# Optimization experiments

Hardware: AMD Instinct MI355X
Metric: run time of the kernel (lower is better)

Reference implementation:

```python
import jax, jax.numpy as jnp
import numpy as np

REG_WEIGHT = 1e-4
N_LAYERS = 3


def setup_inputs() -> dict:
    key = jax.random.key(0)
    ks = jax.random.split(key, 7)
    n_users, n_items, d = 100000, 50000, 64
    E, B = 1600000, 4096
    return {
        "user_table": jax.random.normal(ks[0], (n_users, d), dtype=jnp.float32) * 0.01,
        "item_table": jax.random.normal(ks[1], (n_items, d), dtype=jnp.float32) * 0.01,
        "edge_u": jax.random.randint(ks[2], (E,), 0, n_users, dtype=jnp.int32),
        "edge_i": jax.random.randint(ks[3], (E,), 0, n_items, dtype=jnp.int32),
        "users": jax.random.randint(ks[4], (B,), 0, n_users, dtype=jnp.int32),
        "pos_items": jax.random.randint(ks[5], (B,), 0, n_items, dtype=jnp.int32),
        "neg_items": jax.random.randint(ks[6], (B,), 0, n_items, dtype=jnp.int32),
    }


def _lightgcn_embeddings(user_table, item_table, edge_u, edge_i):
    n_users, n_items = user_table.shape[0], item_table.shape[0]
    N = n_users + n_items
    E = edge_u.shape[0]
    ones = jnp.ones((E,), dtype=user_table.dtype)
    # symmetric normalization D^{-1/2} A D^{-1/2} on the bipartite graph
    deg_u = jax.ops.segment_sum(ones, edge_u, num_segments=n_users)
    deg_i = jax.ops.segment_sum(ones, edge_i, num_segments=n_items)
    w = jax.lax.rsqrt(jnp.maximum(deg_u[edge_u] * deg_i[edge_i], 1.0))
    # symmetric edge list over the stacked [users; items] node set
    rows = jnp.concatenate([edge_u, edge_i + n_users])
    cols = jnp.concatenate([edge_i + n_users, edge_u])
    vals = jnp.concatenate([w, w])[:, None]

    x = jnp.concatenate([user_table, item_table], axis=0)  # [N, d]
    acc = x
    for _ in range(N_LAYERS):
        x = jax.ops.segment_sum(x[cols] * vals, rows, num_segments=N)
        acc = acc + x
    final = acc / jnp.asarray(N_LAYERS + 1, dtype=x.dtype)
    return final[:n_users], final[n_users:]


def reference(user_table, item_table, edge_u, edge_i, users, pos_items, neg_items):
    user_emb_all, item_emb_all = _lightgcn_embeddings(user_table, item_table, edge_u, edge_i)
    u_emb = user_emb_all[users]
    pos_i_emb = item_emb_all[pos_items]
    neg_i_emb = item_emb_all[neg_items]
    pos_scores = jnp.sum(u_emb * pos_i_emb, axis=-1)
    neg_scores = jnp.sum(u_emb * neg_i_emb, axis=-1)
    # L2 regularization on the layer-0 (table) embeddings
    u0 = user_table[users]
    p0 = item_table[pos_items]
    n0 = item_table[neg_items]
    reg_loss = REG_WEIGHT * (jnp.sum(u0 * u0) + jnp.sum(p0 * p0) + jnp.sum(n0 * n0))
    reg_loss = reg_loss / users.shape[0]
    return pos_scores, neg_scores, reg_loss
```

## Files before the change

### kernel.cpp

```cpp
#include <hip/hip_runtime.h>
#include <hip/hip_fp16.h>

#define THREADS 256
#define BIN_C 4096
#define NBMAX 400
#define CAP 4608
#define SH_U 8
#define SH_I 7
#define CPAD 16
#define T_TILES 8
#define TSH_U 13
#define TSH_I 14

__global__ void bin_kernel(const int* __restrict__ eu, const int* __restrict__ ei,
                           int* __restrict__ bcnt_u, int* __restrict__ bcnt_i,
                           int* __restrict__ binu, int* __restrict__ bini,
                           int E, int nbu, int nbi) {
    __shared__ int hist_u[NBMAX], hist_i[NBMAX];
    __shared__ int base_u[NBMAX], base_i[NBMAX];
    int tid = threadIdx.x;
    int e0 = blockIdx.x * BIN_C;
    if (e0 >= E) return;
    int cnt = min(BIN_C, E - e0);

    for (int b = tid; b < NBMAX; b += THREADS) { hist_u[b] = 0; hist_i[b] = 0; }
    __syncthreads();

    int u[16], v[16];
    #pragma unroll
    for (int j = 0; j < 16; ++j) {
        int k = tid + j * THREADS;
        if (k < cnt) { u[j] = eu[e0 + k]; v[j] = ei[e0 + k]; }
        else         { u[j] = -1; v[j] = -1; }
    }
    #pragma unroll
    for (int j = 0; j < 16; ++j) {
        if (u[j] >= 0) {
            atomicAdd(&hist_u[u[j] >> SH_U], 1);
            atomicAdd(&hist_i[v[j] >> SH_I], 1);
        }
    }
    __syncthreads();
    for (int b = tid; b < NBMAX; b += THREADS) {
        int cu = hist_u[b], ci = hist_i[b];
        base_u[b] = (cu > 0 && b < nbu) ? atomicAdd(&bcnt_u[(size_t)b * CPAD], cu) : 0;
        base_i[b] = (ci > 0 && b < nbi) ? atomicAdd(&bcnt_i[(size_t)b * CPAD], ci) : 0;
        hist_u[b] = 0; hist_i[b] = 0;
    }
    __syncthreads();
    #pragma unroll
    for (int j = 0; j < 16; ++j) {
        if (u[j] >= 0) {
            int bu = u[j] >> SH_U;
            int pu = base_u[bu] + atomicAdd(&hist_u[bu], 1);
            if (pu < CAP) binu[(size_t)bu * CAP + pu] = ((u[j] & 255) << 16) | v[j];
            int bi = v[j] >> SH_I;
            int pi = base_i[bi] + atomicAdd(&hist_i[bi], 1);
            if (pi < CAP) bini[(size_t)bi * CAP + pi] = ((v[j] & 127) << 17) | u[j];
        }
    }
}

__global__ void bucket_off(const int* __restrict__ bcnt, int* __restrict__ bo,
                           int* __restrict__ cursor, int nb, int pad) {
    int idx = blockIdx.x * blockDim.x + threadIdx.x;
    int lane = threadIdx.x & 63;
    int d = 0;
    if (idx < nb) d = min(bcnt[(size_t)idx * CPAD], CAP) + pad;
    int s = d;
    #pragma unroll
    for (int ofs = 1; ofs < 64; ofs <<= 1) {
        int t = __shfl_up(s, ofs);
        if (lane >= ofs) s += t;
    }
    int total = __shfl(s, 63);
    int base = 0;
    if (lane == 63) base = atomicAdd(cursor, total);
    base = __shfl(base, 63);
    if (idx < nb) bo[idx] = base + s - d;
}

__global__ void place(const int* __restrict__ bcnt_u, const int* __restrict__ bcnt_i,
                      const int* __restrict__ bo_u, const int* __restrict__ bo_i,
                      const int* __restrict__ binu, const int* __restrict__ bini,
                      int* __restrict__ offu, int* __restrict__ offi,
                      int* __restrict__ du, int* __restrict__ di,
                      float* __restrict__ rsdu, float* __restrict__ rsdi,
                      int* __restrict__ entu, int* __restrict__ enti,
                      int nbu, int nU, int nI) {
    __shared__ int stash[CAP];
    __shared__ int bin_cnt[THREADS * T_TILES];
    __shared__ int scan[THREADS];
    __shared__ int node_base[THREADS];
    int b = blockIdx.x;
    bool isU = (b < nbu);
    const int* bin; int base_node, nn, count, bob;
    int *off, *deg, *ent; float* rsd;
    int losh, tsh, lomask;
    if (isU) {
        bin = binu + (size_t)b * CAP;
        base_node = b << SH_U; nn = min(256, nU - base_node);
        count = min(bcnt_u[(size_t)b * CPAD], CAP); bob = bo_u[b];
        off = offu; deg = du; rsd = rsdu; ent = entu;
        losh = 16; tsh = TSH_U; lomask = 0xFFFF;
    } else {
        int b2 = b - nbu;
        bin = bini + (size_t)b2 * CAP;
        base_node = b2 << SH_I; nn = min(128, nI - base_node);
        count = min(bcnt_i[(size_t)b2 * CPAD], CAP); bob = bo_i[b2];
        off = offi; deg = di; rsd = rsdi; ent = enti;
        losh = 17; tsh = TSH_I; lomask = 0x1FFFF;
    }
    int tid = threadIdx.x;
    #pragma unroll
    for (int t = 0; t < T_TILES; ++t) bin_cnt[tid + t * THREADS] = 0;
    __syncthreads();
    for (int k = tid; k < count; k += THREADS) {
        int p = bin[k];
        stash[k] = p;
        int key = ((p >> losh) << 3) | ((p & lomask) >> tsh);
        atomicAdd(&bin_cnt[key], 1);
    }
    __syncthreads();
    int c = 0;
    {
        int base = tid * T_TILES;
        #pragma unroll
        for (int t = 0; t < T_TILES; ++t) {
            int v = bin_cnt[base + t];
            bin_cnt[base + t] = c;
            c += v;
        }
    }
    int seg = (c + 15) & ~15;
    scan[tid] = seg;
    __syncthreads();
    #pragma unroll
    for (int ofs = 1; ofs < THREADS; ofs <<= 1) {
        int t = (tid >= ofs) ? scan[tid - ofs] : 0;
        __syncthreads();
        scan[tid] += t;
        __syncthreads();
    }
    int excl = scan[tid] - seg;
    node_base[tid] = excl;
    if (tid < nn) {
        off[base_node + tid] = bob + excl;
        deg[base_node + tid] = c;
        rsd[base_node + tid] = rsqrtf(fmaxf((float)c, 1.0f));
    }
    __syncthreads();
    #pragma unroll
    for (int t = 0; t < T_TILES; ++t) {
        int k = tid + t * THREADS;
        bin_cnt[k] += node_base[k >> 3];
    }
    __syncthreads();
    for (int k = tid; k < count; k += THREADS) {
        int p = stash[k];
        int key = ((p >> losh) << 3) | ((p & lomask) >> tsh);
        int sl = atomicAdd(&bin_cnt[key], 1);
        ent[bob + sl] = p & lomask;
    }
}

__global__ void conv16(const float* __restrict__ src, __half* __restrict__ dst, int n4) {
    int stride = gridDim.x * blockDim.x;
    for (int i = blockIdx.x * blockDim.x + threadIdx.x; i < n4; i += stride) {
        float4 v = *reinterpret_cast<const float4*>(src + (size_t)i * 4);
        __half2 h0 = __float22half2_rn(make_float2(v.x, v.y));
        __half2 h1 = __float22half2_rn(make_float2(v.z, v.w));
        uint2 st;
        st.x = *reinterpret_cast<unsigned*>(&h0);
        st.y = *reinterpret_cast<unsigned*>(&h1);
        *reinterpret_cast<uint2*>(dst + (size_t)i * 4) = st;
    }
}

__global__ void prop16(const __half* __restrict__ x,
                       const int* __restrict__ offu, const int* __restrict__ offi,
                       const int* __restrict__ du, const int* __restrict__ di,
                       const float* __restrict__ rsdu, const float* __restrict__ rsdi,
                       const int* __restrict__ entu, const int* __restrict__ enti,
                       __half* __restrict__ y, int nU, int N) {
    int node = blockIdx.x * (THREADS >> 3) + (threadIdx.x >> 3);
    int lane = threadIdx.x & 7;
    if (node >= N) return;
    const int* ent; const __half* src; const float* rsdn;
    int beg, dg; float rs;
    if (node < nU) {
        beg = offu[node]; dg = du[node]; rs = rsdu[node];
        ent = entu; src = x + ((size_t)nU << 6); rsdn = rsdi;
    } else {
        int i = node - nU;
        beg = offi[i]; dg = di[i]; rs = rsdi[i];
        ent = enti; src = x; rsdn = rsdu;
    }
    float a0=0,a1=0,a2=0,a3=0,a4=0,a5=0,a6=0,a7=0;
    for (int k0 = 0; k0 < dg; k0 += 8) {
        int me = (k0 + lane < dg) ? ent[beg + k0 + lane] : 0;
        #pragma unroll
        for (int j = 0; j < 8; ++j) {
            if (k0 + j < dg) {
                int nbr = __shfl(me, j, 8);
                float w = rsdn[nbr];
                uint4 r = *reinterpret_cast<const uint4*>(src + ((size_t)nbr << 6) + (lane << 3));
                __half2 h0 = *reinterpret_cast<__half2*>(&r.x);
                __half2 h1 = *reinterpret_cast<__half2*>(&r.y);
                __half2 h2 = *reinterpret_cast<__half2*>(&r.z);
                __half2 h3 = *reinterpret_cast<__half2*>(&r.w);
                float2 f0 = __half22float2(h0), f1 = __half22float2(h1);
                float2 f2 = __half22float2(h2), f3 = __half22float2(h3);
                a0 += w * f0.x; a1 += w * f0.y; a2 += w * f1.x; a3 += w * f1.y;
                a4 += w * f2.x; a5 += w * f2.y; a6 += w * f3.x; a7 += w * f3.y;
            }
        }
    }
    __half2 o0 = __float22half2_rn(make_float2(a0 * rs, a1 * rs));
    __half2 o1 = __float22half2_rn(make_float2(a2 * rs, a3 * rs));
    __half2 o2 = __float22half2_rn(make_float2(a4 * rs, a5 * rs));
    __half2 o3 = __float22half2_rn(make_float2(a6 * rs, a7 * rs));
    uint4 st;
    st.x = *reinterpret_cast<unsigned*>(&o0);
    st.y = *reinterpret_cast<unsigned*>(&o1);
    st.z = *reinterpret_cast<unsigned*>(&o2);
    st.w = *reinterpret_cast<unsigned*>(&o3);
    *reinterpret_cast<uint4*>(y + ((size_t)node << 6) + (lane << 3)) = st;
}

__global__ void prop_sel(const __half* __restrict__ x,
                         const int* __restrict__ users, const int* __restrict__ pos,
                         const int* __restrict__ neg,
                         const int* __restrict__ offu, const int* __restrict__ offi,
                         const int* __restrict__ du, const int* __restrict__ di,
                         const float* __restrict__ rsdu, const float* __restrict__ rsdi,
                         const int* __restrict__ entu, const int* __restrict__ enti,
                         float* __restrict__ sel, int B, int nU) {
    int r = blockIdx.x * (THREADS >> 3) + (threadIdx.x >> 3);
    int lane = threadIdx.x & 7;
    if (r >= 3 * B) return;
    int which = r / B, b = r - which * B;
    const int* ent; const __half* src; const float* rsdn;
    int beg, dg; float rs;
    if (which == 0) {
        int u = users[b];
        beg = offu[u]; dg = du[u]; rs = rsdu[u];
        ent = entu; src = x + ((size_t)nU << 6); rsdn = rsdi;
    } else {
        int i = (which == 1) ? pos[b] : neg[b];
        beg = offi[i]; dg = di[i]; rs = rsdi[i];
        ent = enti; src = x; rsdn = rsdu;
    }
    float a0=0,a1=0,a2=0,a3=0,a4=0,a5=0,a6=0,a7=0;
    for (int k0 = 0; k0 < dg; k0 += 8) {
        int me = (k0 + lane < dg) ? ent[beg + k0 + lane] : 0;
        #pragma unroll
        for (int j = 0; j < 8; ++j) {
            if (k0 + j < dg) {
                int nbr = __shfl(me, j, 8);
                float w = rsdn[nbr];
                uint4 rv = *reinterpret_cast<const uint4*>(src + ((size_t)nbr << 6) + (lane << 3));
                __half2 h0 = *reinterpret_cast<__half2*>(&rv.x);
                __half2 h1 = *reinterpret_cast<__half2*>(&rv.y);
                __half2 h2 = *reinterpret_cast<__half2*>(&rv.z);
                __half2 h3 = *reinterpret_cast<__half2*>(&rv.w);
                float2 f0 = __half22float2(h0), f1 = __half22float2(h1);
                float2 f2 = __half22float2(h2), f3 = __half22float2(h3);
                a0 += w * f0.x; a1 += w * f0.y; a2 += w * f1.x; a3 += w * f1.y;
                a4 += w * f2.x; a5 += w * f2.y; a6 += w * f3.x; a7 += w * f3.y;
            }
        }
    }
    float* s = sel + ((size_t)r << 6) + (lane << 3);
    float4 d0 = *reinterpret_cast<float4*>(s);
    float4 d1 = *reinterpret_cast<float4*>(s + 4);
    d0.x += rs * a0; d0.y += rs * a1; d0.z += rs * a2; d0.w += rs * a3;
    d1.x += rs * a4; d1.y += rs * a5; d1.z += rs * a6; d1.w += rs * a7;
    *reinterpret_cast<float4*>(s) = d0;
    *reinterpret_cast<float4*>(s + 4) = d1;
}

__global__ void sel_init(const float* __restrict__ ut, const float* __restrict__ it,
                         const int* __restrict__ users, const int* __restrict__ pos,
                         const int* __restrict__ neg, float* __restrict__ sel, int B) {
    int r = blockIdx.x * (THREADS >> 4) + (threadIdx.x >> 4);
    int t = threadIdx.x & 15;
    if (r >= 3 * B) return;
    int which = r / B, b = r - which * B;
    const float* base; int idx;
    if (which == 0)      { base = ut; idx = users[b]; }
    else if (which == 1) { base = it; idx = pos[b]; }
    else                 { base = it; idx = neg[b]; }
    float4 v = *reinterpret_cast<const float4*>(base + ((size_t)idx << 6) + t * 4);
    *reinterpret_cast<float4*>(sel + ((size_t)r << 6) + t * 4) = v;
}

__global__ void sel_acc16(const __half* __restrict__ x,
                          const int* __restrict__ users, const int* __restrict__ pos,
                          const int* __restrict__ neg, float* __restrict__ sel, int B, int nU) {
    int r = blockIdx.x * (THREADS >> 3) + (threadIdx.x >> 3);
    int lane = threadIdx.x & 7;
    if (r >= 3 * B) return;
    int which = r / B, b = r - which * B;
    size_t row;
    if (which == 0)      row = (size_t)users[b];
    else if (which == 1) row = (size_t)nU + pos[b];
    else                 row = (size_t)nU + neg[b];
    uint4 rv = *reinterpret_cast<const uint4*>(x + (row << 6) + (lane << 3));
    __half2 h0 = *reinterpret_cast<__half2*>(&rv.x);
    __half2 h1 = *reinterpret_cast<__half2*>(&rv.y);
    __half2 h2 = *reinterpret_cast<__half2*>(&rv.z);
    __half2 h3 = *reinterpret_cast<__half2*>(&rv.w);
    float2 f0 = __half22float2(h0), f1 = __half22float2(h1);
    float2 f2 = __half22float2(h2), f3 = __half22float2(h3);
    float* s = sel + ((size_t)r << 6) + (lane << 3);
    float4 d0 = *reinterpret_cast<float4*>(s);
    float4 d1 = *reinterpret_cast<float4*>(s + 4);
    d0.x += f0.x; d0.y += f0.y; d0.z += f1.x; d0.w += f1.y;
    d1.x += f2.x; d1.y += f2.y; d1.z += f3.x; d1.w += f3.y;
    *reinterpret_cast<float4*>(s) = d0;
    *reinterpret_cast<float4*>(s + 4) = d1;
}

__global__ void score(const float* __restrict__ sel, float* __restrict__ out, int B) {
    int b = blockIdx.x * (THREADS >> 6) + (threadIdx.x >> 6);
    int lane = threadIdx.x & 63;
    if (b >= B) return;
    float u = sel[((size_t)b << 6) + lane];
    float p = sel[((size_t)(B + b) << 6) + lane];
    float n = sel[((size_t)(2 * B + b) << 6) + lane];
    float ps = u * p, ns = u * n;
    for (int ofs = 32; ofs; ofs >>= 1) {
        ps += __shfl_down(ps, ofs);
        ns += __shfl_down(ns, ofs);
    }
    if (lane == 0) {
        out[b]     = ps * (1.0f / 16.0f);
        out[B + b] = ns * (1.0f / 16.0f);
    }
}

__global__ void regk(const float* __restrict__ ut, const float* __restrict__ it,
                     const int* __restrict__ users, const int* __restrict__ pos,
                     const int* __restrict__ neg,
                     float* __restrict__ out_reg, int B, float scale) {
    int total = 3 * B * 64;
    float s = 0.f;
    int stride = gridDim.x * blockDim.x;
    for (int idx = blockIdx.x * blockDim.x + threadIdx.x; idx < total; idx += stride) {
        int r = idx >> 6, d = idx & 63;
        int which = r / B, b = r - which * B;
        float v;
        if (which == 0)      v = ut[((size_t)users[b] << 6) + d];
        else if (which == 1) v = it[((size_t)pos[b] << 6) + d];
        else                 v = it[((size_t)neg[b] << 6) + d];
        s += v * v;
    }
    for (int ofs = 32; ofs; ofs >>= 1) s += __shfl_down(s, ofs);
    __shared__ float sh[4];
    int lane = threadIdx.x & 63, wid = threadIdx.x >> 6;
    if (lane == 0) sh[wid] = s;
    __syncthreads();
    if (threadIdx.x == 0) {
        float tot = 0.f;
        for (int i = 0; i < (int)(blockDim.x >> 6); ++i) tot += sh[i];
        atomicAdd(out_reg, tot * scale);
    }
}

extern "C" void kernel_launch(void* const* d_in, const int* in_sizes, int n_in,
                              void* d_out, int out_size, void* d_ws, size_t ws_size,
                              hipStream_t stream) {
    const float* ut   = (const float*)d_in[0];
    const float* it   = (const float*)d_in[1];
    const int* eu     = (const int*)d_in[2];
    const int* ei     = (const int*)d_in[3];
    const int* users  = (const int*)d_in[4];
    const int* pos    = (const int*)d_in[5];
    const int* neg    = (const int*)d_in[6];
    int nU = in_sizes[0] / 64;
    int nI = in_sizes[1] / 64;
    int E  = in_sizes[2];
    int B  = in_sizes[4];
    int N  = nU + nI;
    float* out = (float*)d_out;

    int nbu = (nU + 255) >> SH_U;
    int nbi = (nI + 127) >> SH_I;

    char* ws = (char*)d_ws;
    size_t cursor = 0;
    auto alloc = [&](size_t bytes) -> void* {
        cursor = (cursor + 255) & ~(size_t)255;
        void* p = ws + cursor;
        cursor += bytes;
        return p;
    };
    int*   bcnt_u = (int*)alloc((size_t)nbu * CPAD * 4);
    int*   bcnt_i = (int*)alloc((size_t)nbi * CPAD * 4);
    int*   curs   = (int*)alloc(2 * 4);
    size_t zero_span = cursor;
    int*   bo_u = (int*)alloc((size_t)nbu * 4);
    int*   bo_i = (int*)alloc((size_t)nbi * 4);
    int*   binu = (int*)alloc((size_t)nbu * CAP * 4);
    int*   bini = (int*)alloc((size_t)nbi * CAP * 4);
    int*   offu = (int*)alloc((size_t)nU * 4);
    int*   offi = (int*)alloc((size_t)nI * 4);
    int*   du   = (int*)alloc((size_t)nU * 4);
    int*   di   = (int*)alloc((size_t)nI * 4);
    float* rsdu = (float*)alloc((size_t)nU * 4);
    float* rsdi = (float*)alloc((size_t)nI * 4);
    int*   entu = (int*)alloc(((size_t)E + (size_t)nbu * 256 * 16) * 4);
    int*   enti = (int*)alloc(((size_t)E + (size_t)nbi * 128 * 16) * 4);
    __half* xA  = (__half*)alloc((size_t)N * 64 * 2);
    __half* xB  = (__half*)alloc((size_t)N * 64 * 2);
    float* sel  = (float*)alloc((size_t)3 * B * 64 * 4);

    hipMemsetAsync(d_ws, 0, zero_span, stream);
    hipMemsetAsync(out + 2 * B, 0, sizeof(float), stream);

    conv16<<<2048, THREADS, 0, stream>>>(ut, xA, nU * 16);
    conv16<<<2048, THREADS, 0, stream>>>(it, xA + ((size_t)nU << 6), nI * 16);

    int nchunks = (E + BIN_C - 1) / BIN_C;
    bin_kernel<<<nchunks, THREADS, 0, stream>>>(eu, ei, bcnt_u, bcnt_i, binu, bini, E, nbu, nbi);
    bucket_off<<<(nbu + THREADS - 1) / THREADS, THREADS, 0, stream>>>(bcnt_u, bo_u, curs, nbu, 256 * 16);
    bucket_off<<<(nbi + THREADS - 1) / THREADS, THREADS, 0, stream>>>(bcnt_i, bo_i, curs + 1, nbi, 128 * 16);
    place<<<nbu + nbi, THREADS, 0, stream>>>(bcnt_u, bcnt_i, bo_u, bo_i, binu, bini,
                                             offu, offi, du, di, rsdu, rsdi, entu, enti,
                                             nbu, nU, nI);

    int gridSel16 = (3 * B * 8 + THREADS - 1) / THREADS;
    sel_init<<<(3 * B + 15) / 16, THREADS, 0, stream>>>(ut, it, users, pos, neg, sel, B);

    int gridProp = (N * 8 + THREADS - 1) / THREADS;
    prop16<<<gridProp, THREADS, 0, stream>>>(xA, offu, offi, du, di, rsdu, rsdi, entu, enti, xB, nU, N);
    sel_acc16<<<gridSel16, THREADS, 0, stream>>>(xB, users, pos, neg, sel, B, nU);
    prop16<<<gridProp, THREADS, 0, stream>>>(xB, offu, offi, du, di, rsdu, rsdi, entu, enti, xA, nU, N);
    sel_acc16<<<gridSel16, THREADS, 0, stream>>>(xA, users, pos, neg, sel, B, nU);
    prop_sel<<<gridSel16, THREADS, 0, stream>>>(xA, users, pos, neg, offu, offi, du, di,
                                                rsdu, rsdi, entu, enti, sel, B, nU);

    score<<<(B + 3) / 4, THREADS, 0, stream>>>(sel, out, B);
    regk<<<256, THREADS, 0, stream>>>(ut, it, users, pos, neg, out + 2 * B, B, 1e-4f / (float)B);
}
```

Before: 261.3 us.

## Tile neighbor gathers by source range with block-synchronized passes over multiple nodes

The place kernel now records per-node offsets for each of eight source-index tiles. Propagation is rewritten so each 8-lane group handles four nodes and walks the tiles in lockstep, with a block barrier after each tile. The aim is to keep concurrent gathers within one source-index range so they hit cache more often. In exchange it adds tile-offset metadata traffic, more accumulator registers, fewer blocks, and barriers that make groups wait on the slowest node.

```diff
diff --git a/kernel.cpp b/kernel.cpp
--- a/kernel.cpp
+++ b/kernel.cpp
@@ -11,6 +11,7 @@
 #define T_TILES 8
 #define TSH_U 13
 #define TSH_I 14
+#define KNODES 4
 
 __global__ void bin_kernel(const int* __restrict__ eu, const int* __restrict__ ei,
                            int* __restrict__ bcnt_u, int* __restrict__ bcnt_i,
@@ -87,6 +88,7 @@
                       int* __restrict__ du, int* __restrict__ di,
                       float* __restrict__ rsdu, float* __restrict__ rsdi,
                       int* __restrict__ entu, int* __restrict__ enti,
+                      int* __restrict__ tofu, int* __restrict__ tofi,
                       int nbu, int nU, int nI) {
     __shared__ int stash[CAP];
     __shared__ int bin_cnt[THREADS * T_TILES];
@@ -95,20 +97,20 @@
     int b = blockIdx.x;
     bool isU = (b < nbu);
     const int* bin; int base_node, nn, count, bob;
-    int *off, *deg, *ent; float* rsd;
+    int *off, *deg, *ent, *tof; float* rsd;
     int losh, tsh, lomask;
     if (isU) {
         bin = binu + (size_t)b * CAP;
         base_node = b << SH_U; nn = min(256, nU - base_node);
         count = min(bcnt_u[(size_t)b * CPAD], CAP); bob = bo_u[b];
-        off = offu; deg = du; rsd = rsdu; ent = entu;
+        off = offu; deg = du; rsd = rsdu; ent = entu; tof = tofu;
         losh = 16; tsh = TSH_U; lomask = 0xFFFF;
     } else {
         int b2 = b - nbu;
         bin = bini + (size_t)b2 * CAP;
         base_node = b2 << SH_I; nn = min(128, nI - base_node);
         count = min(bcnt_i[(size_t)b2 * CPAD], CAP); bob = bo_i[b2];
-        off = offi; deg = di; rsd = rsdi; ent = enti;
+        off = offi; deg = di; rsd = rsdi; ent = enti; tof = tofi;
         losh = 17; tsh = TSH_I; lomask = 0x1FFFF;
     }
     int tid = threadIdx.x;
@@ -148,6 +150,9 @@
         off[base_node + tid] = bob + excl;
         deg[base_node + tid] = c;
         rsd[base_node + tid] = rsqrtf(fmaxf((float)c, 1.0f));
+        #pragma unroll
+        for (int t = 0; t < T_TILES; ++t)
+            tof[(size_t)(base_node + tid) * T_TILES + t] = bob + excl + bin_cnt[tid * T_TILES + t];
     }
     __syncthreads();
     #pragma unroll
@@ -177,55 +182,83 @@
     }
 }
 
-__global__ void prop16(const __half* __restrict__ x,
-                       const int* __restrict__ offu, const int* __restrict__ offi,
-                       const int* __restrict__ du, const int* __restrict__ di,
-                       const float* __restrict__ rsdu, const float* __restrict__ rsdi,
-                       const int* __restrict__ entu, const int* __restrict__ enti,
-                       __half* __restrict__ y, int nU, int N) {
-    int node = blockIdx.x * (THREADS >> 3) + (threadIdx.x >> 3);
+__global__ __launch_bounds__(THREADS, 4)
+void prop16t(const __half* __restrict__ x,
+             const int* __restrict__ tofu, const int* __restrict__ tofi,
+             const int* __restrict__ offu, const int* __restrict__ offi,
+             const int* __restrict__ du, const int* __restrict__ di,
+             const float* __restrict__ rsdu, const float* __restrict__ rsdi,
+             const int* __restrict__ entu, const int* __restrict__ enti,
+             __half* __restrict__ y, int nU, int N) {
+    int g = threadIdx.x >> 3;
     int lane = threadIdx.x & 7;
-    if (node >= N) return;
-    const int* ent; const __half* src; const float* rsdn;
-    int beg, dg; float rs;
-    if (node < nU) {
-        beg = offu[node]; dg = du[node]; rs = rsdu[node];
-        ent = entu; src = x + ((size_t)nU << 6); rsdn = rsdi;
-    } else {
-        int i = node - nU;
-        beg = offi[i]; dg = di[i]; rs = rsdi[i];
-        ent = enti; src = x; rsdn = rsdu;
-    }
-    float a0=0,a1=0,a2=0,a3=0,a4=0,a5=0,a6=0,a7=0;
-    for (int k0 = 0; k0 < dg; k0 += 8) {
-        int me = (k0 + lane < dg) ? ent[beg + k0 + lane] : 0;
+    int node0 = (blockIdx.x * (THREADS >> 3) + g) * KNODES;
+    const __half* srcI = x + ((size_t)nU << 6);
+    float acc[KNODES][8];
+    #pragma unroll
+    for (int k = 0; k < KNODES; ++k)
         #pragma unroll
-        for (int j = 0; j < 8; ++j) {
-            if (k0 + j < dg) {
-                int nbr = __shfl(me, j, 8);
-                float w = rsdn[nbr];
-                uint4 r = *reinterpret_cast<const uint4*>(src + ((size_t)nbr << 6) + (lane << 3));
-                __half2 h0 = *reinterpret_cast<__half2*>(&r.x);
-                __half2 h1 = *reinterpret_cast<__half2*>(&r.y);
-                __half2 h2 = *reinterpret_cast<__half2*>(&r.z);
-                __half2 h3 = *reinterpret_cast<__half2*>(&r.w);
-                float2 f0 = __half22float2(h0), f1 = __half22float2(h1);
-                float2 f2 = __half22float2(h2), f3 = __half22float2(h3);
-                a0 += w * f0.x; a1 += w * f0.y; a2 += w * f1.x; a3 += w * f1.y;
-                a4 += w * f2.x; a5 += w * f2.y; a6 += w * f3.x; a7 += w * f3.y;
+        for (int j = 0; j < 8; ++j) acc[k][j] = 0.f;
+
+    for (int t = 0; t < T_TILES; ++t) {
+        #pragma unroll
+        for (int k = 0; k < KNODES; ++k) {
+            int node = node0 + k;
+            if (node >= N) continue;
+            const int* ent; const __half* src; const float* rsdn;
+            int s, e;
+            if (node < nU) {
+                const int* tf = tofu + (size_t)node * T_TILES;
+                s = tf[t];
+                e = (t < T_TILES - 1) ? tf[t + 1] : offu[node] + du[node];
+                ent = entu; src = srcI; rsdn = rsdi;
+            } else {
+                int i = node - nU;
+                const int* tf = tofi + (size_t)i * T_TILES;
+                s = tf[t];
+                e = (t < T_TILES - 1) ? tf[t + 1] : offi[i] + di[i];
+                ent = enti; src = x; rsdn = rsdu;
+            }
+            for (int k0 = s; k0 < e; k0 += 8) {
+                int me = (k0 + lane < e) ? ent[k0 + lane] : 0;
+                #pragma unroll
+                for (int j = 0; j < 8; ++j) {
+                    if (k0 + j < e) {
+                        int nbr = __shfl(me, j, 8);
+                        float w = rsdn[nbr];
+                        uint4 r = *reinterpret_cast<const uint4*>(src + ((size_t)nbr << 6) + (lane << 3));
+                        __half2 h0 = *reinterpret_cast<__half2*>(&r.x);
+                        __half2 h1 = *reinterpret_cast<__half2*>(&r.y);
+                        __half2 h2 = *reinterpret_cast<__half2*>(&r.z);
+                        __half2 h3 = *reinterpret_cast<__half2*>(&r.w);
+                        float2 f0 = __half22float2(h0), f1 = __half22float2(h1);
+                        float2 f2 = __half22float2(h2), f3 = __half22float2(h3);
+                        acc[k][0] += w * f0.x; acc[k][1] += w * f0.y;
+                        acc[k][2] += w * f1.x; acc[k][3] += w * f1.y;
+                        acc[k][4] += w * f2.x; acc[k][5] += w * f2.y;
+                        acc[k][6] += w * f3.x; acc[k][7] += w * f3.y;
+                    }
+                }
             }
         }
-    }
-    __half2 o0 = __float22half2_rn(make_float2(a0 * rs, a1 * rs));
-    __half2 o1 = __float22half2_rn(make_float2(a2 * rs, a3 * rs));
-    __half2 o2 = __float22half2_rn(make_float2(a4 * rs, a5 * rs));
-    __half2 o3 = __float22half2_rn(make_float2(a6 * rs, a7 * rs));
-    uint4 st;
-    st.x = *reinterpret_cast<unsigned*>(&o0);
-    st.y = *reinterpret_cast<unsigned*>(&o1);
-    st.z = *reinterpret_cast<unsigned*>(&o2);
-    st.w = *reinterpret_cast<unsigned*>(&o3);
-    *reinterpret_cast<uint4*>(y + ((size_t)node << 6) + (lane << 3)) = st;
+        __syncthreads();
+    }
+    #pragma unroll
+    for (int k = 0; k < KNODES; ++k) {
+        int node = node0 + k;
+        if (node >= N) continue;
+        float rs = (node < nU) ? rsdu[node] : rsdi[node - nU];
+        __half2 o0 = __float22half2_rn(make_float2(acc[k][0] * rs, acc[k][1] * rs));
+        __half2 o1 = __float22half2_rn(make_float2(acc[k][2] * rs, acc[k][3] * rs));
+        __half2 o2 = __float22half2_rn(make_float2(acc[k][4] * rs, acc[k][5] * rs));
+        __half2 o3 = __float22half2_rn(make_float2(acc[k][6] * rs, acc[k][7] * rs));
+        uint4 st;
+        st.x = *reinterpret_cast<unsigned*>(&o0);
+        st.y = *reinterpret_cast<unsigned*>(&o1);
+        st.z = *reinterpret_cast<unsigned*>(&o2);
+        st.w = *reinterpret_cast<unsigned*>(&o3);
+        *reinterpret_cast<uint4*>(y + ((size_t)node << 6) + (lane << 3)) = st;
+    }
 }
 
 __global__ void prop_sel(const __half* __restrict__ x,
@@ -410,6 +443,8 @@
     int*   di   = (int*)alloc((size_t)nI * 4);
     float* rsdu = (float*)alloc((size_t)nU * 4);
     float* rsdi = (float*)alloc((size_t)nI * 4);
+    int*   tofu = (int*)alloc((size_t)nU * T_TILES * 4);
+    int*   tofi = (int*)alloc((size_t)nI * T_TILES * 4);
     int*   entu = (int*)alloc(((size_t)E + (size_t)nbu * 256 * 16) * 4);
     int*   enti = (int*)alloc(((size_t)E + (size_t)nbi * 128 * 16) * 4);
     __half* xA  = (__half*)alloc((size_t)N * 64 * 2);
@@ -428,15 +463,18 @@
     bucket_off<<<(nbi + THREADS - 1) / THREADS, THREADS, 0, stream>>>(bcnt_i, bo_i, curs + 1, nbi, 128 * 16);
     place<<<nbu + nbi, THREADS, 0, stream>>>(bcnt_u, bcnt_i, bo_u, bo_i, binu, bini,
                                              offu, offi, du, di, rsdu, rsdi, entu, enti,
-                                             nbu, nU, nI);
+                                             tofu, tofi, nbu, nU, nI);
 
     int gridSel16 = (3 * B * 8 + THREADS - 1) / THREADS;
     sel_init<<<(3 * B + 15) / 16, THREADS, 0, stream>>>(ut, it, users, pos, neg, sel, B);
 
-    int gridProp = (N * 8 + THREADS - 1) / THREADS;
-    prop16<<<gridProp, THREADS, 0, stream>>>(xA, offu, offi, du, di, rsdu, rsdi, entu, enti, xB, nU, N);
+    int nodesPerBlock = (THREADS >> 3) * KNODES;
+    int gridProp = (N + nodesPerBlock - 1) / nodesPerBlock;
+    prop16t<<<gridProp, THREADS, 0, stream>>>(xA, tofu, tofi, offu, offi, du, di,
+                                              rsdu, rsdi, entu, enti, xB, nU, N);
     sel_acc16<<<gridSel16, THREADS, 0, stream>>>(xB, users, pos, neg, sel, B, nU);
-    prop16<<<gridProp, THREADS, 0, stream>>>(xB, offu, offi, du, di, rsdu, rsdi, entu, enti, xA, nU, N);
+    prop16t<<<gridProp, THREADS, 0, stream>>>(xB, tofu, tofi, offu, offi, du, di,
+                                              rsdu, rsdi, entu, enti, xA, nU, N);
     sel_acc16<<<gridSel16, THREADS, 0, stream>>>(xA, users, pos, neg, sel, B, nU);
     prop_sel<<<gridSel16, THREADS, 0, stream>>>(xA, users, pos, neg, offu, offi, du, di,
                                                 rsdu, rsdi, entu, enti, sel, B, nU);
```

Result: slower. 396.3 us (+51.7%).

## Fuse small kernels: in-place bucket offsets, merged conversion, selection+reg, final accumulate

Applied to the files above, without the earlier changes.

Removes the bucket_off kernels by having each place block take its base offset through a global atomic after a wave-shuffle scan, which also replaces the shared-memory Hillis-Steele scan. It merges the two conv16 launches into one, folds the regularisation sum into the selection-init kernel, and folds the last sel_acc16 into prop_sel. The goal is fewer launches and less barrier overhead. In exchange, bucket offsets now follow block completion order rather than bucket order, which changes the edge layout but not correctness. It also adds one atomic per wave for the reg sum.

```diff
diff --git a/kernel.cpp b/kernel.cpp
--- a/kernel.cpp
+++ b/kernel.cpp
@@ -61,53 +61,35 @@
     }
 }
 
-__global__ void bucket_off(const int* __restrict__ bcnt, int* __restrict__ bo,
-                           int* __restrict__ cursor, int nb, int pad) {
-    int idx = blockIdx.x * blockDim.x + threadIdx.x;
-    int lane = threadIdx.x & 63;
-    int d = 0;
-    if (idx < nb) d = min(bcnt[(size_t)idx * CPAD], CAP) + pad;
-    int s = d;
-    #pragma unroll
-    for (int ofs = 1; ofs < 64; ofs <<= 1) {
-        int t = __shfl_up(s, ofs);
-        if (lane >= ofs) s += t;
-    }
-    int total = __shfl(s, 63);
-    int base = 0;
-    if (lane == 63) base = atomicAdd(cursor, total);
-    base = __shfl(base, 63);
-    if (idx < nb) bo[idx] = base + s - d;
-}
-
 __global__ void place(const int* __restrict__ bcnt_u, const int* __restrict__ bcnt_i,
-                      const int* __restrict__ bo_u, const int* __restrict__ bo_i,
                       const int* __restrict__ binu, const int* __restrict__ bini,
                       int* __restrict__ offu, int* __restrict__ offi,
                       int* __restrict__ du, int* __restrict__ di,
                       float* __restrict__ rsdu, float* __restrict__ rsdi,
                       int* __restrict__ entu, int* __restrict__ enti,
+                      int* __restrict__ curs,
                       int nbu, int nU, int nI) {
     __shared__ int stash[CAP];
     __shared__ int bin_cnt[THREADS * T_TILES];
-    __shared__ int scan[THREADS];
     __shared__ int node_base[THREADS];
+    __shared__ int wsum[4];
+    __shared__ int bob_sh;
     int b = blockIdx.x;
     bool isU = (b < nbu);
-    const int* bin; int base_node, nn, count, bob;
+    const int* bin; int base_node, nn, count;
     int *off, *deg, *ent; float* rsd;
     int losh, tsh, lomask;
     if (isU) {
         bin = binu + (size_t)b * CAP;
         base_node = b << SH_U; nn = min(256, nU - base_node);
-        count = min(bcnt_u[(size_t)b * CPAD], CAP); bob = bo_u[b];
+        count = min(bcnt_u[(size_t)b * CPAD], CAP);
         off = offu; deg = du; rsd = rsdu; ent = entu;
         losh = 16; tsh = TSH_U; lomask = 0xFFFF;
     } else {
         int b2 = b - nbu;
         bin = bini + (size_t)b2 * CAP;
         base_node = b2 << SH_I; nn = min(128, nI - base_node);
-        count = min(bcnt_i[(size_t)b2 * CPAD], CAP); bob = bo_i[b2];
+        count = min(bcnt_i[(size_t)b2 * CPAD], CAP);
         off = offi; deg = di; rsd = rsdi; ent = enti;
         losh = 17; tsh = TSH_I; lomask = 0x1FFFF;
     }
@@ -133,16 +115,23 @@
         }
     }
     int seg = (c + 15) & ~15;
-    scan[tid] = seg;
-    __syncthreads();
-    #pragma unroll
-    for (int ofs = 1; ofs < THREADS; ofs <<= 1) {
-        int t = (tid >= ofs) ? scan[tid - ofs] : 0;
-        __syncthreads();
-        scan[tid] += t;
-        __syncthreads();
-    }
-    int excl = scan[tid] - seg;
+    int lane = tid & 63, wid = tid >> 6;
+    int inc = seg;
+    #pragma unroll
+    for (int ofs = 1; ofs < 64; ofs <<= 1) {
+        int t = __shfl_up(inc, ofs);
+        if (lane >= ofs) inc += t;
+    }
+    if (lane == 63) wsum[wid] = inc;
+    __syncthreads();
+    int wofs = 0;
+    #pragma unroll
+    for (int w = 0; w < 4; ++w) wofs += (w < wid) ? wsum[w] : 0;
+    int incl = inc + wofs;
+    int excl = incl - seg;
+    if (tid == THREADS - 1) bob_sh = atomicAdd(&curs[isU ? 0 : 1], incl);
+    __syncthreads();
+    int bob = bob_sh;
     node_base[tid] = excl;
     if (tid < nn) {
         off[base_node + tid] = bob + excl;
@@ -164,10 +153,12 @@
     }
 }
 
-__global__ void conv16(const float* __restrict__ src, __half* __restrict__ dst, int n4) {
+__global__ void conv16all(const float* __restrict__ ut, const float* __restrict__ it,
+                          __half* __restrict__ dst, int nU16, int ntot16) {
     int stride = gridDim.x * blockDim.x;
-    for (int i = blockIdx.x * blockDim.x + threadIdx.x; i < n4; i += stride) {
-        float4 v = *reinterpret_cast<const float4*>(src + (size_t)i * 4);
+    for (int i = blockIdx.x * blockDim.x + threadIdx.x; i < ntot16; i += stride) {
+        const float* src = (i < nU16) ? (ut + (size_t)i * 4) : (it + (size_t)(i - nU16) * 4);
+        float4 v = *reinterpret_cast<const float4*>(src);
         __half2 h0 = __float22half2_rn(make_float2(v.x, v.y));
         __half2 h1 = __float22half2_rn(make_float2(v.z, v.w));
         uint2 st;
@@ -228,28 +219,30 @@
     *reinterpret_cast<uint4*>(y + ((size_t)node << 6) + (lane << 3)) = st;
 }
 
-__global__ void prop_sel(const __half* __restrict__ x,
-                         const int* __restrict__ users, const int* __restrict__ pos,
-                         const int* __restrict__ neg,
-                         const int* __restrict__ offu, const int* __restrict__ offi,
-                         const int* __restrict__ du, const int* __restrict__ di,
-                         const float* __restrict__ rsdu, const float* __restrict__ rsdi,
-                         const int* __restrict__ entu, const int* __restrict__ enti,
-                         float* __restrict__ sel, int B, int nU) {
+__global__ void prop_sel_acc(const __half* __restrict__ x,
+                             const int* __restrict__ users, const int* __restrict__ pos,
+                             const int* __restrict__ neg,
+                             const int* __restrict__ offu, const int* __restrict__ offi,
+                             const int* __restrict__ du, const int* __restrict__ di,
+                             const float* __restrict__ rsdu, const float* __restrict__ rsdi,
+                             const int* __restrict__ entu, const int* __restrict__ enti,
+                             float* __restrict__ sel, int B, int nU) {
     int r = blockIdx.x * (THREADS >> 3) + (threadIdx.x >> 3);
     int lane = threadIdx.x & 7;
     if (r >= 3 * B) return;
     int which = r / B, b = r - which * B;
     const int* ent; const __half* src; const float* rsdn;
-    int beg, dg; float rs;
+    int beg, dg; float rs; size_t selfrow;
     if (which == 0) {
         int u = users[b];
         beg = offu[u]; dg = du[u]; rs = rsdu[u];
         ent = entu; src = x + ((size_t)nU << 6); rsdn = rsdi;
+        selfrow = (size_t)u << 6;
     } else {
         int i = (which == 1) ? pos[b] : neg[b];
         beg = offi[i]; dg = di[i]; rs = rsdi[i];
         ent = enti; src = x; rsdn = rsdu;
+        selfrow = (size_t)(nU + i) << 6;
     }
     float a0=0,a1=0,a2=0,a3=0,a4=0,a5=0,a6=0,a7=0;
     for (int k0 = 0; k0 < dg; k0 += 8) {
@@ -271,28 +264,45 @@
             }
         }
     }
+    uint4 rv = *reinterpret_cast<const uint4*>(x + selfrow + (lane << 3));
+    __half2 h0 = *reinterpret_cast<__half2*>(&rv.x);
+    __half2 h1 = *reinterpret_cast<__half2*>(&rv.y);
+    __half2 h2 = *reinterpret_cast<__half2*>(&rv.z);
+    __half2 h3 = *reinterpret_cast<__half2*>(&rv.w);
+    float2 s0 = __half22float2(h0), s1 = __half22float2(h1);
+    float2 s2 = __half22float2(h2), s3 = __half22float2(h3);
     float* s = sel + ((size_t)r << 6) + (lane << 3);
     float4 d0 = *reinterpret_cast<float4*>(s);
     float4 d1 = *reinterpret_cast<float4*>(s + 4);
-    d0.x += rs * a0; d0.y += rs * a1; d0.z += rs * a2; d0.w += rs * a3;
-    d1.x += rs * a4; d1.y += rs * a5; d1.z += rs * a6; d1.w += rs * a7;
+    d0.x += s0.x + rs * a0; d0.y += s0.y + rs * a1;
+    d0.z += s1.x + rs * a2; d0.w += s1.y + rs * a3;
+    d1.x += s2.x + rs * a4; d1.y += s2.y + rs * a5;
+    d1.z += s3.x + rs * a6; d1.w += s3.y + rs * a7;
     *reinterpret_cast<float4*>(s) = d0;
     *reinterpret_cast<float4*>(s + 4) = d1;
 }
 
-__global__ void sel_init(const float* __restrict__ ut, const float* __restrict__ it,
-                         const int* __restrict__ users, const int* __restrict__ pos,
-                         const int* __restrict__ neg, float* __restrict__ sel, int B) {
+__global__ void selreg(const float* __restrict__ ut, const float* __restrict__ it,
+                       const int* __restrict__ users, const int* __restrict__ pos,
+                       const int* __restrict__ neg,
+                       float* __restrict__ sel, float* __restrict__ out_reg,
+                       int B, float scale) {
     int r = blockIdx.x * (THREADS >> 4) + (threadIdx.x >> 4);
     int t = threadIdx.x & 15;
-    if (r >= 3 * B) return;
-    int which = r / B, b = r - which * B;
-    const float* base; int idx;
-    if (which == 0)      { base = ut; idx = users[b]; }
-    else if (which == 1) { base = it; idx = pos[b]; }
-    else                 { base = it; idx = neg[b]; }
-    float4 v = *reinterpret_cast<const float4*>(base + ((size_t)idx << 6) + t * 4);
-    *reinterpret_cast<float4*>(sel + ((size_t)r << 6) + t * 4) = v;
+    float ssq = 0.f;
+    if (r < 3 * B) {
+        int which = r / B, b = r - which * B;
+        const float* base; int idx;
+        if (which == 0)      { base = ut; idx = users[b]; }
+        else if (which == 1) { base = it; idx = pos[b]; }
+        else                 { base = it; idx = neg[b]; }
+        float4 v = *reinterpret_cast<const float4*>(base + ((size_t)idx << 6) + t * 4);
+        *reinterpret_cast<float4*>(sel + ((size_t)r << 6) + t * 4) = v;
+        ssq = v.x * v.x + v.y * v.y + v.z * v.z + v.w * v.w;
+    }
+    #pragma unroll
+    for (int ofs = 32; ofs; ofs >>= 1) ssq += __shfl_down(ssq, ofs);
+    if ((threadIdx.x & 63) == 0) atomicAdd(out_reg, ssq * scale);
 }
 
 __global__ void sel_acc16(const __half* __restrict__ x,
@@ -340,34 +350,6 @@
     }
 }
 
-__global__ void regk(const float* __restrict__ ut, const float* __restrict__ it,
-                     const int* __restrict__ users, const int* __restrict__ pos,
-                     const int* __restrict__ neg,
-                     float* __restrict__ out_reg, int B, float scale) {
-    int total = 3 * B * 64;
-    float s = 0.f;
-    int stride = gridDim.x * blockDim.x;
-    for (int idx = blockIdx.x * blockDim.x + threadIdx.x; idx < total; idx += stride) {
-        int r = idx >> 6, d = idx & 63;
-        int which = r / B, b = r - which * B;
-        float v;
-        if (which == 0)      v = ut[((size_t)users[b] << 6) + d];
-        else if (which == 1) v = it[((size_t)pos[b] << 6) + d];
-        else                 v = it[((size_t)neg[b] << 6) + d];
-        s += v * v;
-    }
-    for (int ofs = 32; ofs; ofs >>= 1) s += __shfl_down(s, ofs);
-    __shared__ float sh[4];
-    int lane = threadIdx.x & 63, wid = threadIdx.x >> 6;
-    if (lane == 0) sh[wid] = s;
-    __syncthreads();
-    if (threadIdx.x == 0) {
-        float tot = 0.f;
-        for (int i = 0; i < (int)(blockDim.x >> 6); ++i) tot += sh[i];
-        atomicAdd(out_reg, tot * scale);
-    }
-}
-
 extern "C" void kernel_launch(void* const* d_in, const int* in_sizes, int n_in,
                               void* d_out, int out_size, void* d_ws, size_t ws_size,
                               hipStream_t stream) {
@@ -400,8 +382,6 @@
     int*   bcnt_i = (int*)alloc((size_t)nbi * CPAD * 4);
     int*   curs   = (int*)alloc(2 * 4);
     size_t zero_span = cursor;
-    int*   bo_u = (int*)alloc((size_t)nbu * 4);
-    int*   bo_i = (int*)alloc((size_t)nbi * 4);
     int*   binu = (int*)alloc((size_t)nbu * CAP * 4);
     int*   bini = (int*)alloc((size_t)nbi * CAP * 4);
     int*   offu = (int*)alloc((size_t)nU * 4);
@@ -419,28 +399,24 @@
     hipMemsetAsync(d_ws, 0, zero_span, stream);
     hipMemsetAsync(out + 2 * B, 0, sizeof(float), stream);
 
-    conv16<<<2048, THREADS, 0, stream>>>(ut, xA, nU * 16);
-    conv16<<<2048, THREADS, 0, stream>>>(it, xA + ((size_t)nU << 6), nI * 16);
+    conv16all<<<2048, THREADS, 0, stream>>>(ut, it, xA, nU * 16, N * 16);
 
     int nchunks = (E + BIN_C - 1) / BIN_C;
     bin_kernel<<<nchunks, THREADS, 0, stream>>>(eu, ei, bcnt_u, bcnt_i, binu, bini, E, nbu, nbi);
-    bucket_off<<<(nbu + THREADS - 1) / THREADS, THREADS, 0, stream>>>(bcnt_u, bo_u, curs, nbu, 256 * 16);
-    bucket_off<<<(nbi + THREADS - 1) / THREADS, THREADS, 0, stream>>>(bcnt_i, bo_i, curs + 1, nbi, 128 * 16);
-    place<<<nbu + nbi, THREADS, 0, stream>>>(bcnt_u, bcnt_i, bo_u, bo_i, binu, bini,
+    place<<<nbu + nbi, THREADS, 0, stream>>>(bcnt_u, bcnt_i, binu, bini,
                                              offu, offi, du, di, rsdu, rsdi, entu, enti,
-                                             nbu, nU, nI);
+                                             curs, nbu, nU, nI);
+
+    selreg<<<(3 * B + 15) / 16, THREADS, 0, stream>>>(ut, it, users, pos, neg, sel,
+                                                      out + 2 * B, B, 1e-4f / (float)B);
 
     int gridSel16 = (3 * B * 8 + THREADS - 1) / THREADS;
-    sel_init<<<(3 * B + 15) / 16, THREADS, 0, stream>>>(ut, it, users, pos, neg, sel, B);
-
     int gridProp = (N * 8 + THREADS - 1) / THREADS;
     prop16<<<gridProp, THREADS, 0, stream>>>(xA, offu, offi, du, di, rsdu, rsdi, entu, enti, xB, nU, N);
     sel_acc16<<<gridSel16, THREADS, 0, stream>>>(xB, users, pos, neg, sel, B, nU);
     prop16<<<gridProp, THREADS, 0, stream>>>(xB, offu, offi, du, di, rsdu, rsdi, entu, enti, xA, nU, N);
-    sel_acc16<<<gridSel16, THREADS, 0, stream>>>(xA, users, pos, neg, sel, B, nU);
-    prop_sel<<<gridSel16, THREADS, 0, stream>>>(xA, users, pos, neg, offu, offi, du, di,
-                                                rsdu, rsdi, entu, enti, sel, B, nU);
+    prop_sel_acc<<<gridSel16, THREADS, 0, stream>>>(xA, users, pos, neg, offu, offi, du, di,
+                                                    rsdu, rsdi, entu, enti, sel, B, nU);
 
     score<<<(B + 3) / 4, THREADS, 0, stream>>>(sel, out, B);
-    regk<<<256, THREADS, 0, stream>>>(ut, it, users, pos, neg, out + 2 * B, B, 1e-4f / (float)B);
-}
+}
```

After: 284.7 us. 9.0% more time.
